# Kernel optimization log

Hardware: AMD Instinct MI355X
Metric: run time of the kernel (lower is better)

Reference implementation:

```python
import jax, jax.numpy as jnp
import numpy as np

NUM_CODE = 8192
CODE_DIM = 256


def setup_inputs() -> dict:
    key = jax.random.key(0)
    k1, k2 = jax.random.split(key)
    z_e = jax.random.normal(k1, (16, CODE_DIM, 32, 32), dtype=jnp.float32)
    span = 1.0 / NUM_CODE
    codebook = jax.random.uniform(k2, (NUM_CODE, CODE_DIM), dtype=jnp.float32,
                                  minval=-span, maxval=span)
    return {"z_e": z_e, "codebook": codebook}


def reference(z_e, codebook):
    # NCHW -> NHWC
    z = jnp.transpose(z_e, (0, 2, 3, 1))  # [B,H,W,D]
    B, H, W, D = z.shape
    flat = z.reshape(-1, D)  # [N,D]
    cb = jax.lax.stop_gradient(codebook)
    # squared L2 distances without materializing [N,K,D] diff tensor
    z2 = jnp.sum(flat * flat, axis=1, keepdims=True)          # [N,1]
    c2 = jnp.sum(cb * cb, axis=1)                              # [K]
    dist = z2 - 2.0 * (flat @ cb.T) + c2[None, :]              # [N,K]
    indices = jnp.argmin(dist, axis=1)                         # [N]
    z_q_flat = cb[indices]                                     # [N,D]
    z_q = z_q_flat.reshape(B, H, W, D)
    # straight-through estimator
    z_q = z + jax.lax.stop_gradient(z_q - z)
    idx = indices.reshape(B, H, W)
    z_q = jnp.transpose(z_q, (0, 3, 1, 2))  # NHWC -> NCHW
    return z_q, idx
```

## Files before the change

kernel.cpp:

```cpp
#include <hip/hip_runtime.h>

typedef __attribute__((ext_vector_type(4))) unsigned int u32x4;
typedef __attribute__((ext_vector_type(4))) int i32x4;

union I16 { u32x4 u; i32x4 i; };

#define SA_INV   (127.0f / 12.0f)
#define SB_INV   (127.0f * 8192.0f)
#define INV_SASB ((127.0 * 127.0 * 8192.0) / 12.0)
#define WI       4500
#define FINF     3.4e38f

__device__ __forceinline__ int q8(float x, float s) {
    int q = (int)__builtin_rintf(x * s);
    return q < -127 ? -127 : (q > 127 ? 127 : q);
}

__global__ __launch_bounds__(256)
void prep_all(const float* __restrict__ z, const float* __restrict__ cb,
              u32x4* __restrict__ ahi, float* __restrict__ zt,
              float* __restrict__ z2f, float* __restrict__ c2,
              unsigned int* __restrict__ ibt, u32x4* __restrict__ bstr) {
    __shared__ double pzbuf[32 * 9];
    __shared__ float tile[32 * 257];
    int tid = threadIdx.x;
    if (blockIdx.x < 512) {
        float* t16 = tile;
        float* pc = (float*)pzbuf;
        int ct = blockIdx.x;
        int cl = tid >> 4, dseg = tid & 15;
        const float* src = cb + (size_t)(ct * 16 + cl) * 256 + dseg * 16;
        float s = 0.f;
#pragma unroll
        for (int i = 0; i < 16; ++i) { float v = src[i]; t16[cl * 257 + dseg * 16 + i] = v; s += v * v; }
        pc[cl * 17 + dseg] = s;
        __syncthreads();
        if (tid < 16) {
            float t = 0.f;
#pragma unroll
            for (int i = 0; i < 16; ++i) t += pc[tid * 17 + i];
            int code = ct * 16 + tid;
            c2[code] = t;
            int ib = (int)__builtin_rintf(t * (float)INV_SASB);
            ibt[code] = (((unsigned int)(ib + 262144)) << 6) | (unsigned int)((code >> 4) & 31);
        }
        int l = tid & 63, j = tid >> 6;
        int code_l = l & 15, k0 = j * 64 + ((l >> 4) << 4);
        u32x4 v;
#pragma unroll
        for (int d = 0; d < 4; ++d) {
            unsigned int wv = 0;
#pragma unroll
            for (int bb = 0; bb < 4; ++bb) {
                int q = q8(t16[code_l * 257 + k0 + d * 4 + bb], SB_INV);
                wv |= ((unsigned int)(q & 255)) << (8 * bb);
            }
            v[d] = wv;
        }
        bstr[(size_t)(ct * 4 + j) * 64 + l] = v;
    } else {
        int bh = blockIdx.x - 512;
        int b = bh >> 5, h = bh & 31;
        for (int e = tid; e < 8192; e += 256) {
            int d = e >> 5, w = e & 31;
            tile[w * 257 + d] = z[((size_t)(b * 256 + d) * 32 + h) * 32 + w];
        }
        __syncthreads();
        for (int e = tid; e < 8192; e += 256) {
            int w = e >> 8, d = e & 255;
            zt[(size_t)(bh * 32 + w) * 256 + d] = tile[w * 257 + d];
        }
        {
            int w = tid >> 3, seg = tid & 7;
            double s = 0.0;
#pragma unroll
            for (int d = 0; d < 32; ++d) { double v = (double)tile[w * 257 + seg * 32 + d]; s += v * v; }
            pzbuf[w * 9 + seg] = s;
        }
        __syncthreads();
        if (tid < 32) {
            double s = 0.0;
#pragma unroll
            for (int seg = 0; seg < 8; ++seg) s += pzbuf[tid * 9 + seg];
            z2f[bh * 32 + tid] = (float)s;
        }
        for (int o = tid; o < 512; o += 256) {
            int l = o & 63, j = (o >> 6) & 3, tt = o >> 8;
            int wp = tt * 16 + (l & 15);
            int k0 = j * 64 + ((l >> 4) << 4);
            u32x4 v;
#pragma unroll
            for (int d = 0; d < 4; ++d) {
                unsigned int wv = 0;
#pragma unroll
                for (int bb = 0; bb < 4; ++bb) {
                    int q = q8(-2.0f * tile[wp * 257 + k0 + d * 4 + bb], SA_INV);
                    wv |= ((unsigned int)(q & 255)) << (8 * bb);
                }
                v[d] = wv;
            }
            ahi[(size_t)bh * 512 + o] = v;
        }
    }
}

__global__ __launch_bounds__(256)
void vq_main(const u32x4* __restrict__ ahi4, const u32x4* __restrict__ bstr,
             const unsigned int* __restrict__ ibt,
             unsigned int* __restrict__ cd, int* __restrict__ ci) {
    int tid = threadIdx.x;
    int wid = tid >> 6, lane = tid & 63;
    int stripe = blockIdx.x & 15;
    int rg = blockIdx.x >> 4;
    int colc = lane & 15;
    int rt0 = rg * 8 + wid * 2;

    I16 ah[2][4];
#pragma unroll
    for (int rt = 0; rt < 2; ++rt)
#pragma unroll
        for (int j = 0; j < 4; ++j)
            ah[rt][j].u = ahi4[((size_t)(rt0 + rt) * 4 + j) * 64 + lane];

    unsigned int m1[8], m2[8];
#pragma unroll
    for (int s = 0; s < 8; ++s) { m1[s] = 0xFFFFFFFFu; m2[s] = 0xFFFFFFFFu; }

    const u32x4* p0 = bstr + (size_t)stripe * 8192 + lane;
    const u32x4* p1 = p0 + 256;
    const unsigned int* ip = ibt + stripe * 512 + colc;
    i32x4 zc = (i32x4){0, 0, 0, 0};

    I16 bfA[4], bfB[4];
    unsigned int ibA, ibB;
#pragma unroll
    for (int j = 0; j < 4; ++j) bfA[j].u = p0[j * 64];
    ibA = ip[0];

    auto tilework = [&](const I16 (&bf)[4], unsigned int ibv) {
        i32x4 acc0, acc1;
        acc0 = __builtin_amdgcn_mfma_i32_16x16x64_i8(ah[0][0].i, bf[0].i, zc, 0, 0, 0);
        acc1 = __builtin_amdgcn_mfma_i32_16x16x64_i8(ah[1][0].i, bf[0].i, zc, 0, 0, 0);
#pragma unroll
        for (int j = 1; j < 4; ++j) {
            acc0 = __builtin_amdgcn_mfma_i32_16x16x64_i8(ah[0][j].i, bf[j].i, acc0, 0, 0, 0);
            acc1 = __builtin_amdgcn_mfma_i32_16x16x64_i8(ah[1][j].i, bf[j].i, acc1, 0, 0, 0);
        }
#pragma unroll
        for (int s = 0; s < 8; ++s) {
            unsigned int av = (unsigned int)((s < 4) ? acc0[s & 3] : acc1[s & 3]);
            unsigned int key, tmp;
            asm("v_lshl_add_u32 %0, %4, 6, %5\n\t"
                "v_max_u32 %1, %0, %2\n\t"
                "v_min_u32 %3, %3, %1\n\t"
                "v_min_u32 %2, %2, %0"
                : "=&v"(key), "=&v"(tmp), "+v"(m1[s]), "+v"(m2[s])
                : "v"(av), "v"(ibv));
        }
    };

    for (int t = 0; t < 32; t += 2) {
#pragma unroll
        for (int j = 0; j < 4; ++j) bfB[j].u = p1[j * 64];
        ibB = ip[(t + 1) * 16];
        tilework(bfA, ibA);
        if (t + 2 < 32) {
            p0 += 512;
#pragma unroll
            for (int j = 0; j < 4; ++j) bfA[j].u = p0[j * 64];
            ibA = ip[(t + 2) * 16];
        }
        tilework(bfB, ibB);
        p1 += 512;
    }

#pragma unroll
    for (int s = 0; s < 8; ++s) {
        int rt = s >> 2, r = s & 3;
        int row = (rt0 + rt) * 16 + (lane >> 4) * 4 + r;
        unsigned int v0 = m1[s], v1 = m2[s];
        int c0 = stripe * 512 + (int)(v0 & 63) * 16 + colc;
        int c1 = stripe * 512 + (int)(v1 & 63) * 16 + colc;
        int obase = (row * 16 + stripe) * 3;
#pragma unroll
        for (int k = 0; k < 3; ++k) {
            unsigned int bv; int bi;
            if (v1 < v0) { bv = v1; bi = c1; } else { bv = v0; bi = c0; }
#pragma unroll
            for (int mm = 1; mm < 16; mm <<= 1) {
                unsigned int ov = __shfl_xor(bv, mm, 64);
                int oi = __shfl_xor(bi, mm, 64);
                if (ov < bv || (ov == bv && oi < bi)) { bv = ov; bi = oi; }
            }
            if (colc == k) { cd[obase + k] = bv; ci[obase + k] = bi; }
            if (bi == c0) v0 = 0xFFFFFFFFu;
            if (bi == c1) v1 = 0xFFFFFFFFu;
        }
    }
}

__global__ __launch_bounds__(256)
void refine(const float* __restrict__ zt, const float* __restrict__ z2f,
            const float* __restrict__ cb, const float* __restrict__ c2,
            const unsigned int* __restrict__ cd, const int* __restrict__ ci,
            float* __restrict__ out, int* __restrict__ idxi) {
    int wid = threadIdx.x >> 6, lane = threadIdx.x & 63;
    int n = blockIdx.x * 4 + wid;
    float zq[4];
#pragma unroll
    for (int q = 0; q < 4; ++q) zq[q] = zt[(size_t)n * 256 + q * 64 + lane];
    float z2v = z2f[n];

    unsigned int kd = 0xFFFFFFFFu; int civ = 0;
    if (lane < 48) { kd = cd[n * 48 + lane]; civ = ci[n * 48 + lane]; }
    unsigned int rm = kd;
#pragma unroll
    for (int m = 32; m >= 1; m >>= 1) {
        unsigned int o = __shfl_xor(rm, m, 64);
        rm = o < rm ? o : rm;
    }
    bool active = (lane < 48) && ((kd >> 6) <= (rm >> 6) + WI);
    unsigned long long mask = __ballot(active);
    float bestd = FINF; int besti = 0x7fffffff;
    while (mask) {
        int k = __ffsll(mask) - 1;
        mask &= mask - 1;
        int cidx = __shfl(civ, k, 64);
        const float* crow = cb + (size_t)cidx * 256;
        double dot = 0.0;
#pragma unroll
        for (int q = 0; q < 4; ++q)
            dot += (double)zq[q] * (double)crow[q * 64 + lane];
#pragma unroll
        for (int m = 32; m >= 1; m >>= 1) dot += __shfl_xor(dot, m, 64);
        float Mf = (float)dot;
        float d1 = z2v - 2.0f * Mf;
        float d2 = d1 + c2[cidx];
        if (d2 < bestd || (d2 == bestd && cidx < besti)) { bestd = d2; besti = cidx; }
    }
    if (lane == 0) {
        idxi[n] = besti;
        out[4194304 + n] = (float)besti;
    }
}

__global__ void gather_out(const float* __restrict__ cb,
                           const int* __restrict__ idxi,
                           float* __restrict__ out) {
    __shared__ float tile[32][257];
    __shared__ int sidx[32];
    int b = blockIdx.x >> 5, h = blockIdx.x & 31;
    int tid = threadIdx.x;
    if (tid < 32) sidx[tid] = idxi[(b * 32 + h) * 32 + tid];
    __syncthreads();
    for (int e = tid; e < 8192; e += 256) {
        int w = e >> 8, d = e & 255;
        tile[w][d] = cb[(size_t)sidx[w] * 256 + d];
    }
    __syncthreads();
    for (int e = tid; e < 8192; e += 256) {
        int d = e >> 5, w = e & 31;
        out[(((size_t)b * 256 + d) * 32 + h) * 32 + w] = tile[w][d];
    }
}

extern "C" void kernel_launch(void* const* d_in, const int* in_sizes, int n_in,
                              void* d_out, int out_size, void* d_ws, size_t ws_size,
                              hipStream_t stream) {
    const float* z  = (const float*)d_in[0];
    const float* cb = (const float*)d_in[1];
    float* out = (float*)d_out;
    char* w = (char*)d_ws;
    u32x4* ahi  = (u32x4*)(w);
    u32x4* bstr = (u32x4*)(w + 4194304);
    float* zt   = (float*)(w + 6291456);
    float* c2   = (float*)(w + 23068672);
    unsigned int* ibt = (unsigned int*)(w + 23101440);
    float* z2f  = (float*)(w + 23134208);
    unsigned int* cd = (unsigned int*)(w + 23199744);
    int*   ci   = (int*)(w + 26345472);
    int*   idxi = (int*)(w);

    prep_all<<<1024, 256, 0, stream>>>(z, cb, ahi, zt, z2f, c2, ibt, bstr);
    vq_main<<<2048, 256, 0, stream>>>(ahi, bstr, ibt, cd, ci);
    refine<<<4096, 256, 0, stream>>>(zt, z2f, cb, c2, cd, ci, out, idxi);
    gather_out<<<512, 256, 0, stream>>>(cb, idxi, out);
}
```

Before: 161.4 us.

## Stage codebook tiles through LDS with async global_load_lds double buffering

Each wave used to load the codebook B-fragments straight from global memory into registers, so all four waves in a block fetched the same data separately. Now the block loads each pair of tiles cooperatively into LDS with global_load_lds into a double buffer, and stages the index table in LDS too. Waves then read their fragments from LDS. This cuts redundant global traffic per block, at the cost of a __syncthreads per iteration and LDS read latency inside the MFMA loop.

```diff
diff --git a/kernel.cpp b/kernel.cpp
--- a/kernel.cpp
+++ b/kernel.cpp
@@ -14,6 +14,12 @@
 __device__ __forceinline__ int q8(float x, float s) {
     int q = (int)__builtin_rintf(x * s);
     return q < -127 ? -127 : (q > 127 ? 127 : q);
+}
+
+__device__ __forceinline__ void glds16(const u32x4* g, u32x4* l) {
+    __builtin_amdgcn_global_load_lds(
+        (const __attribute__((address_space(1))) unsigned int*)g,
+        (__attribute__((address_space(3))) unsigned int*)l, 16, 0, 0);
 }
 
 __global__ __launch_bounds__(256)
@@ -108,6 +114,8 @@
 void vq_main(const u32x4* __restrict__ ahi4, const u32x4* __restrict__ bstr,
              const unsigned int* __restrict__ ibt,
              unsigned int* __restrict__ cd, int* __restrict__ ci) {
+    __shared__ u32x4 lbuf[2][2][256];
+    __shared__ unsigned int libt[512];
     int tid = threadIdx.x;
     int wid = tid >> 6, lane = tid & 63;
     int stripe = blockIdx.x & 15;
@@ -115,6 +123,8 @@
     int colc = lane & 15;
     int rt0 = rg * 8 + wid * 2;
 
+    for (int e = tid; e < 512; e += 256) libt[e] = ibt[stripe * 512 + e];
+
     I16 ah[2][4];
 #pragma unroll
     for (int rt = 0; rt < 2; ++rt)
@@ -126,16 +136,14 @@
 #pragma unroll
     for (int s = 0; s < 8; ++s) { m1[s] = 0xFFFFFFFFu; m2[s] = 0xFFFFFFFFu; }
 
-    const u32x4* p0 = bstr + (size_t)stripe * 8192 + lane;
-    const u32x4* p1 = p0 + 256;
-    const unsigned int* ip = ibt + stripe * 512 + colc;
+    const u32x4* gsrc = bstr + (size_t)stripe * 8192 + tid;
+    int ldsbase = wid << 6;
+
+    glds16(gsrc,       &lbuf[0][0][ldsbase]);
+    glds16(gsrc + 256, &lbuf[0][1][ldsbase]);
+    __syncthreads();
+
     i32x4 zc = (i32x4){0, 0, 0, 0};
-
-    I16 bfA[4], bfB[4];
-    unsigned int ibA, ibB;
-#pragma unroll
-    for (int j = 0; j < 4; ++j) bfA[j].u = p0[j * 64];
-    ibA = ip[0];
 
     auto tilework = [&](const I16 (&bf)[4], unsigned int ibv) {
         i32x4 acc0, acc1;
@@ -159,19 +167,23 @@
         }
     };
 
-    for (int t = 0; t < 32; t += 2) {
-#pragma unroll
-        for (int j = 0; j < 4; ++j) bfB[j].u = p1[j * 64];
-        ibB = ip[(t + 1) * 16];
-        tilework(bfA, ibA);
-        if (t + 2 < 32) {
-            p0 += 512;
-#pragma unroll
-            for (int j = 0; j < 4; ++j) bfA[j].u = p0[j * 64];
-            ibA = ip[(t + 2) * 16];
-        }
-        tilework(bfB, ibB);
-        p1 += 512;
+    int cur = 0;
+    for (int p = 0; p < 16; ++p) {
+        if (p < 15) {
+            const u32x4* gs = gsrc + (size_t)(p + 1) * 512;
+            glds16(gs,       &lbuf[cur ^ 1][0][ldsbase]);
+            glds16(gs + 256, &lbuf[cur ^ 1][1][ldsbase]);
+        }
+#pragma unroll
+        for (int tt = 0; tt < 2; ++tt) {
+            I16 bf[4];
+#pragma unroll
+            for (int j = 0; j < 4; ++j) bf[j].u = lbuf[cur][tt][j * 64 + lane];
+            unsigned int ibv = libt[(p * 2 + tt) * 16 + colc];
+            tilework(bf, ibv);
+        }
+        __syncthreads();
+        cur ^= 1;
     }
 
 #pragma unroll
```

After: 158.6 us. About the same (-1.7%).
